# Kernel optimization log

Measured on AMD Instinct MI355X. Metric: run time of the kernel, lower is better.

## Reference

```python
import jax, jax.numpy as jnp
import numpy as np

PI_APPROX = 3.14  # the original module uses 3.14, not math.pi
FPS = 30.0        # hard-coded sampling rate in calc_hr_torch


def setup_inputs() -> dict:
    key = jax.random.key(0)
    x = jax.random.normal(key, (4096, 4096), dtype=jnp.float32)
    return {"x": x}


def reference(x) -> jnp.ndarray:
    test_n, sig_length = x.shape
    # mean-subtract each signal (over last dim)
    x = x - jnp.mean(x, axis=-1, keepdims=True)

    # custom_fft: DFT over dim 0 (size test_n), O(N^2) via trig matmuls
    N = test_n
    n = jnp.arange(N, dtype=jnp.float32)[:, None]  # [N,1]
    k = jnp.arange(N, dtype=jnp.float32)[None, :]  # [1,N]
    ang = (-2.0 * PI_APPROX / N) * (k * n)         # [N,N]
    real_part = jnp.matmul(jnp.cos(ang), x)        # [N, sig_length]
    imag_part = jnp.matmul(jnp.sin(ang), x)

    # custom_rfft: keep non-negative frequencies along dim 0
    half = N // 2 + 1 if N % 2 == 0 else (N + 1) // 2
    real_part = real_part[:half]
    imag_part = imag_part[:half]

    Ns = sig_length
    freq = jnp.arange(Ns, dtype=jnp.float32) / (Ns / FPS)  # [sig_length]
    amplitude = jnp.sqrt(real_part ** 2 + imag_part ** 2) / Ns  # [half, sig_length]
    hr_list = freq[jnp.argmax(amplitude, axis=-1)] * 60.0       # [half]
    return hr_list
```

## Files before the change

kernel.cpp:

```cpp
#include <hip/hip_runtime.h>
#include <cmath>

typedef _Float16 f16;
typedef _Float16 f16x8 __attribute__((ext_vector_type(8)));
typedef float f32x4 __attribute__((ext_vector_type(4)));
typedef unsigned long long u64;

#define M_OUT 2049
#define NDIM 4096
#define MPAD 2112
#define CW ((float)(-2.0 * 3.14 / 4096.0))

static const size_t WS_MEAN  = 0;
static const size_t WS_CELLS = 16384;
static const size_t WS_TBL   = 40960;
static const size_t A_ELEMS  = (size_t)MPAD * NDIM;
static const size_t X_ELEMS  = (size_t)NDIM * NDIM;
static const size_t WS_XTBL  = WS_TBL + 4 * A_ELEMS * sizeof(f16);
static const size_t WS_FULL_END = WS_XTBL + 2 * X_ELEMS * sizeof(f16);
static const size_t WS_MID_END  = WS_TBL + 4 * A_ELEMS * sizeof(f16);

#define AS1 __attribute__((address_space(1)))
#define AS3 __attribute__((address_space(3)))
__device__ __forceinline__ void async_copy16(const void* gsrc, void* ldst) {
    __builtin_amdgcn_global_load_lds((const AS1 unsigned int*)gsrc,
                                     (AS3 unsigned int*)ldst, 16, 0, 0);
}

__device__ __forceinline__ void split_f16(float v, f16& hi, f16& lo) {
    hi = (f16)v;
    lo = (f16)((v - (float)hi) * 64.0f);
}

__global__ void mean_kernel(const float* __restrict__ x, float* __restrict__ meanv,
                            u64* __restrict__ cells) {
    if (blockIdx.x < 9) {
        int i = blockIdx.x * 256 + threadIdx.x;
        if (i < M_OUT) cells[i] = 0ull;
    }
    const int row = blockIdx.x;
    const float4* xr = (const float4*)(x + (size_t)row * NDIM);
    float s = 0.f;
    for (int i = threadIdx.x; i < NDIM / 4; i += 256) {
        float4 v = xr[i];
        s += (v.x + v.y) + (v.z + v.w);
    }
    for (int off = 32; off; off >>= 1) s += __shfl_down(s, off);
    __shared__ float ps[4];
    if ((threadIdx.x & 63) == 0) ps[threadIdx.x >> 6] = s;
    __syncthreads();
    if (threadIdx.x == 0) {
        float t = (ps[0] + ps[1]) + (ps[2] + ps[3]);
        meanv[row] = t * (1.0f / 4096.0f);
    }
}

__global__ void fill_tables_cm(const float* __restrict__ x, const float* __restrict__ meanv,
                               f16* __restrict__ atbl, f16* __restrict__ xtbl) {
    const int c = blockIdx.x;
    if (blockIdx.y < 9) {
        const int m = blockIdx.y * 256 + threadIdx.x;
        if (m >= MPAD) return;
        const bool valid = (m < M_OUT);
        f16x8 chv, clv, shv, slv;
        for (int j = 0; j < 8; ++j) {
            float cc = 0.f, ss = 0.f;
            if (valid) {
                int kk = c * 8 + j;
                float ang = CW * (float)(m * kk);
                sincosf(ang, &ss, &cc);
            }
            f16 h, l;
            split_f16(cc, h, l); chv[j] = h; clv[j] = l;
            split_f16(ss, h, l); shv[j] = h; slv[j] = l;
        }
        size_t idx = ((size_t)c * MPAD + m) * 8;
        *(f16x8*)(atbl + idx)                 = chv;
        *(f16x8*)(atbl + A_ELEMS + idx)       = clv;
        *(f16x8*)(atbl + 2 * A_ELEMS + idx)   = shv;
        *(f16x8*)(atbl + 3 * A_ELEMS + idx)   = slv;
    } else {
        const int n = (blockIdx.y - 9) * 256 + threadIdx.x;
        f16x8 hv, lv;
        for (int j = 0; j < 8; ++j) {
            int k = c * 8 + j;
            float v = x[(size_t)k * NDIM + n] - meanv[k];
            f16 h, l;
            split_f16(v, h, l);
            hv[j] = h; lv[j] = l;
        }
        size_t idx = ((size_t)c * NDIM + n) * 8;
        *(f16x8*)(xtbl + idx)           = hv;
        *(f16x8*)(xtbl + X_ELEMS + idx) = lv;
    }
}

__global__ __launch_bounds__(256, 2) void dft_gemm_cm(
    const f16* __restrict__ atbl, const f16* __restrict__ xtbl,
    u64* __restrict__ cells)
{
    __shared__ alignas(16) f16 sX[3][2][4][128][8];

    const int t = threadIdx.x;
    const int n0 = blockIdx.x * 128;
    const int by = blockIdx.y;

    const int lane = t & 63;
    const int w  = t >> 6;
    const int wm = w >> 1, wn = w & 1;
    const int q  = lane >> 4, ln = lane & 15;

    f32x4 aC0[2][4], aC1[2][4], aS0[2][4], aS1[2][4];

    const int xq0 = w >> 1, xh = w & 1;
    const int xq1 = xq0 + 2;
    const f16* xG0 = xtbl + ((size_t)xq0 * NDIM + n0 + xh * 64 + lane) * 8;
    const f16* xG1 = xtbl + ((size_t)xq1 * NDIM + n0 + xh * 64 + lane) * 8;
    const f16* xG2 = xG0 + X_ELEMS;
    const f16* xG3 = xG1 + X_ELEMS;

    auto stageX = [&](int buf, int kc) {
        const size_t kadv = (size_t)kc * NDIM * 8;
        async_copy16(xG0 + kadv, &sX[buf][0][xq0][xh * 64][0]);
        async_copy16(xG1 + kadv, &sX[buf][0][xq1][xh * 64][0]);
        async_copy16(xG2 + kadv, &sX[buf][1][xq0][xh * 64][0]);
        async_copy16(xG3 + kadv, &sX[buf][1][xq1][xh * 64][0]);
    };

    auto compute = [&](f16x8 (&A)[2][4], int buf) {
        f16x8 bh[4], bl[4];
#pragma unroll
        for (int tn = 0; tn < 4; ++tn) {
            int nl = wn * 64 + tn * 16 + ln;
            bh[tn] = *(const f16x8*)&sX[buf][0][q][nl][0];
            bl[tn] = *(const f16x8*)&sX[buf][1][q][nl][0];
        }
        __builtin_amdgcn_s_setprio(1);
#pragma unroll
        for (int tm = 0; tm < 2; ++tm)
#pragma unroll
            for (int tn = 0; tn < 4; ++tn) {
                aC0[tm][tn] = __builtin_amdgcn_mfma_f32_16x16x32_f16(A[tm][0], bh[tn], aC0[tm][tn], 0, 0, 0);
                aC1[tm][tn] = __builtin_amdgcn_mfma_f32_16x16x32_f16(A[tm][0], bl[tn], aC1[tm][tn], 0, 0, 0);
                aC1[tm][tn] = __builtin_amdgcn_mfma_f32_16x16x32_f16(A[tm][1], bh[tn], aC1[tm][tn], 0, 0, 0);
                aS0[tm][tn] = __builtin_amdgcn_mfma_f32_16x16x32_f16(A[tm][2], bh[tn], aS0[tm][tn], 0, 0, 0);
                aS1[tm][tn] = __builtin_amdgcn_mfma_f32_16x16x32_f16(A[tm][2], bl[tn], aS1[tm][tn], 0, 0, 0);
                aS1[tm][tn] = __builtin_amdgcn_mfma_f32_16x16x32_f16(A[tm][3], bh[tn], aS1[tm][tn], 0, 0, 0);
            }
        __builtin_amdgcn_s_setprio(0);
    };

    f16x8 Aa[2][4], Ab[2][4];

    const int npass = (by == 0) ? 2 : 1;
    for (int pass = 0; pass < npass; ++pass) {
        const int rowBase = (pass == 0) ? by * 64 : 2048;
        __syncthreads();

#pragma unroll
        for (int i = 0; i < 2; ++i)
#pragma unroll
            for (int j = 0; j < 4; ++j) {
                aC0[i][j] = (f32x4){0.f, 0.f, 0.f, 0.f};
                aC1[i][j] = (f32x4){0.f, 0.f, 0.f, 0.f};
                aS0[i][j] = (f32x4){0.f, 0.f, 0.f, 0.f};
                aS1[i][j] = (f32x4){0.f, 0.f, 0.f, 0.f};
            }

        const f16* aBase = atbl + ((size_t)q * MPAD + (rowBase + wm * 32 + ln)) * 8;

        auto loadA = [&](f16x8 (&dst)[2][4], int kc) {
#pragma unroll
            for (int tm = 0; tm < 2; ++tm)
#pragma unroll
                for (int tb = 0; tb < 4; ++tb)
                    dst[tm][tb] = *(const f16x8*)(aBase + (size_t)tb * A_ELEMS
                                  + ((size_t)kc * MPAD + tm * 16) * 8);
        };

        int cur = 0, nxt = 1;
        auto bump = [&]() { cur = nxt; nxt = (nxt == 2) ? 0 : nxt + 1; };

        stageX(0, 0);
        loadA(Aa, 0);

        int kc = 0;
        for (int it = 0; it < 63; ++it) {
            loadA(Ab, kc + 4);
            stageX(nxt, kc + 4);
            asm volatile("s_waitcnt vmcnt(12)" ::: "memory");
            __builtin_amdgcn_s_barrier();
            __builtin_amdgcn_sched_barrier(0);
            compute(Aa, cur);
            bump();
            kc += 4;
            loadA(Aa, kc + 4);
            stageX(nxt, kc + 4);
            asm volatile("s_waitcnt vmcnt(12)" ::: "memory");
            __builtin_amdgcn_s_barrier();
            __builtin_amdgcn_sched_barrier(0);
            compute(Ab, cur);
            bump();
            kc += 4;
        }
        loadA(Ab, kc + 4);
        stageX(nxt, kc + 4);
        asm volatile("s_waitcnt vmcnt(12)" ::: "memory");
        __builtin_amdgcn_s_barrier();
        __builtin_amdgcn_sched_barrier(0);
        compute(Aa, cur);
        bump();
        asm volatile("s_waitcnt vmcnt(0)" ::: "memory");
        __builtin_amdgcn_s_barrier();
        __builtin_amdgcn_sched_barrier(0);
        compute(Ab, cur);

        const float inv64 = 0.015625f;
#pragma unroll
        for (int tm = 0; tm < 2; ++tm) {
#pragma unroll
            for (int r = 0; r < 4; ++r) {
                u64 best = 0ull;
#pragma unroll
                for (int tn = 0; tn < 4; ++tn) {
                    float C = aC0[tm][tn][r] + aC1[tm][tn][r] * inv64;
                    float S = aS0[tm][tn][r] + aS1[tm][tn][r] * inv64;
                    float a2 = C * C + S * S;
                    int col = n0 + wn * 64 + tn * 16 + ln;
                    u64 key = ((u64)__float_as_uint(a2) << 32) | (unsigned)(~col);
                    if (key > best) best = key;
                }
                for (int off = 1; off < 16; off <<= 1) {
                    unsigned hi = (unsigned)(best >> 32), lo = (unsigned)best;
                    unsigned ho = __shfl_xor(hi, off);
                    unsigned lo2 = __shfl_xor(lo, off);
                    u64 o = ((u64)ho << 32) | lo2;
                    if (o > best) best = o;
                }
                if (ln == 0) {
                    int grow = rowBase + wm * 32 + tm * 16 + q * 4 + r;
                    if (grow < M_OUT) atomicMax(cells + grow, best);
                }
            }
        }
    }
}

__global__ void fill_tables_rm(f16* __restrict__ tbl) {
    long long g = (long long)blockIdx.x * 256 + threadIdx.x;
    if (g >= (long long)(MPAD * 512)) return;
    int m  = (int)(g >> 9);
    int kq = ((int)g & 511) * 8;
    bool valid = (m < M_OUT);
    f16x8 chv, clv, shv, slv;
    for (int j = 0; j < 8; ++j) {
        float c = 0.f, s = 0.f;
        if (valid) {
            int kk = kq + j;
            float ang = CW * (float)(m * kk);
            sincosf(ang, &s, &c);
        }
        f16 h, l;
        split_f16(c, h, l); chv[j] = h; clv[j] = l;
        split_f16(s, h, l); shv[j] = h; slv[j] = l;
    }
    size_t idx = (size_t)m * NDIM + kq;
    *(f16x8*)(tbl + idx)               = chv;
    *(f16x8*)(tbl + A_ELEMS + idx)     = clv;
    *(f16x8*)(tbl + 2 * A_ELEMS + idx) = shv;
    *(f16x8*)(tbl + 3 * A_ELEMS + idx) = slv;
}

#define PK 40
__global__ __launch_bounds__(256, 2) void dft_gemm_fb(
    const float* __restrict__ x, const float* __restrict__ meanv,
    const f16* __restrict__ tbl, int useTbl,
    u64* __restrict__ cells)
{
    __shared__ alignas(16) f16 Ach[64][PK];
    __shared__ alignas(16) f16 Acl[64][PK];
    __shared__ alignas(16) f16 Ash[64][PK];
    __shared__ alignas(16) f16 Asl[64][PK];
    __shared__ alignas(16) f16 Xh[128][PK];
    __shared__ alignas(16) f16 Xl[128][PK];

    const int t = threadIdx.x;
    const int n0      = blockIdx.x * 128;
    const int rowBase = blockIdx.y * 64;

    const int am  = t >> 2;
    const int akq = (t & 3) * 8;
    const int xn  = t & 127;
    const int xkh = (t >> 7) * 16;

    const int lane = t & 63;
    const int w  = t >> 6;
    const int wm = w >> 1, wn = w & 1;
    const int q  = lane >> 4, ln = lane & 15;

    f32x4 aC0[2][4], aC1[2][4], aS0[2][4], aS1[2][4];
    for (int i = 0; i < 2; ++i)
        for (int j = 0; j < 4; ++j) {
            aC0[i][j] = (f32x4){0.f, 0.f, 0.f, 0.f};
            aC1[i][j] = (f32x4){0.f, 0.f, 0.f, 0.f};
            aS0[i][j] = (f32x4){0.f, 0.f, 0.f, 0.f};
            aS1[i][j] = (f32x4){0.f, 0.f, 0.f, 0.f};
        }

    const int arow = rowBase + am;
    const bool avalid = (arow < M_OUT);

    for (int k0 = 0; k0 < NDIM; k0 += 32) {
        __syncthreads();
        if (useTbl) {
            size_t idx = (size_t)arow * NDIM + k0 + akq;
            *(f16x8*)&Ach[am][akq] = *(const f16x8*)(tbl + idx);
            *(f16x8*)&Acl[am][akq] = *(const f16x8*)(tbl + A_ELEMS + idx);
            *(f16x8*)&Ash[am][akq] = *(const f16x8*)(tbl + 2 * A_ELEMS + idx);
            *(f16x8*)&Asl[am][akq] = *(const f16x8*)(tbl + 3 * A_ELEMS + idx);
        } else {
            f16x8 chv, clv, shv, slv;
            for (int j = 0; j < 8; ++j) {
                float c = 0.f, s = 0.f;
                if (avalid) {
                    int kk = k0 + akq + j;
                    float ang = CW * (float)(arow * kk);
                    sincosf(ang, &s, &c);
                }
                f16 h, l;
                split_f16(c, h, l); chv[j] = h; clv[j] = l;
                split_f16(s, h, l); shv[j] = h; slv[j] = l;
            }
            *(f16x8*)&Ach[am][akq] = chv;
            *(f16x8*)&Acl[am][akq] = clv;
            *(f16x8*)&Ash[am][akq] = shv;
            *(f16x8*)&Asl[am][akq] = slv;
        }
        {
            const float* xp = x + (size_t)(k0 + xkh) * NDIM + n0 + xn;
            f16x8 h0, h1, l0, l1;
            for (int r = 0; r < 16; ++r) {
                float v = xp[(size_t)r * NDIM] - meanv[k0 + xkh + r];
                f16 hi, lo;
                split_f16(v, hi, lo);
                if (r < 8) { h0[r] = hi; l0[r] = lo; }
                else       { h1[r - 8] = hi; l1[r - 8] = lo; }
            }
            *(f16x8*)&Xh[xn][xkh]     = h0;
            *(f16x8*)&Xh[xn][xkh + 8] = h1;
            *(f16x8*)&Xl[xn][xkh]     = l0;
            *(f16x8*)&Xl[xn][xkh + 8] = l1;
        }
        __syncthreads();
        f16x8 fch[2], fcl[2], fsh[2], fsl[2], bh[4], bl[4];
        for (int tm = 0; tm < 2; ++tm) {
            int ml = wm * 32 + tm * 16 + ln;
            fch[tm] = *(const f16x8*)&Ach[ml][q * 8];
            fcl[tm] = *(const f16x8*)&Acl[ml][q * 8];
            fsh[tm] = *(const f16x8*)&Ash[ml][q * 8];
            fsl[tm] = *(const f16x8*)&Asl[ml][q * 8];
        }
        for (int tn = 0; tn < 4; ++tn) {
            int nl = wn * 64 + tn * 16 + ln;
            bh[tn] = *(const f16x8*)&Xh[nl][q * 8];
            bl[tn] = *(const f16x8*)&Xl[nl][q * 8];
        }
        for (int tm = 0; tm < 2; ++tm)
            for (int tn = 0; tn < 4; ++tn) {
                aC0[tm][tn] = __builtin_amdgcn_mfma_f32_16x16x32_f16(fch[tm], bh[tn], aC0[tm][tn], 0, 0, 0);
                aC1[tm][tn] = __builtin_amdgcn_mfma_f32_16x16x32_f16(fch[tm], bl[tn], aC1[tm][tn], 0, 0, 0);
                aC1[tm][tn] = __builtin_amdgcn_mfma_f32_16x16x32_f16(fcl[tm], bh[tn], aC1[tm][tn], 0, 0, 0);
                aS0[tm][tn] = __builtin_amdgcn_mfma_f32_16x16x32_f16(fsh[tm], bh[tn], aS0[tm][tn], 0, 0, 0);
                aS1[tm][tn] = __builtin_amdgcn_mfma_f32_16x16x32_f16(fsh[tm], bl[tn], aS1[tm][tn], 0, 0, 0);
                aS1[tm][tn] = __builtin_amdgcn_mfma_f32_16x16x32_f16(fsl[tm], bh[tn], aS1[tm][tn], 0, 0, 0);
            }
    }

    const float inv64 = 0.015625f;
    for (int tm = 0; tm < 2; ++tm) {
        for (int r = 0; r < 4; ++r) {
            u64 best = 0ull;
            for (int tn = 0; tn < 4; ++tn) {
                float C = aC0[tm][tn][r] + aC1[tm][tn][r] * inv64;
                float S = aS0[tm][tn][r] + aS1[tm][tn][r] * inv64;
                float a2 = C * C + S * S;
                int col = n0 + wn * 64 + tn * 16 + ln;
                u64 key = ((u64)__float_as_uint(a2) << 32) | (unsigned)(~col);
                if (key > best) best = key;
            }
            for (int off = 1; off < 16; off <<= 1) {
                unsigned hi = (unsigned)(best >> 32), lo = (unsigned)best;
                unsigned ho = __shfl_xor(hi, off);
                unsigned lo2 = __shfl_xor(lo, off);
                u64 o = ((u64)ho << 32) | lo2;
                if (o > best) best = o;
            }
            if (ln == 0) {
                int grow = rowBase + wm * 32 + tm * 16 + q * 4 + r;
                if (grow < M_OUT) atomicMax(cells + grow, best);
            }
        }
    }
}

__global__ void out_kernel(const u64* __restrict__ cells, float* __restrict__ out) {
    int i = blockIdx.x * 256 + threadIdx.x;
    if (i < M_OUT) {
        unsigned col = ~(unsigned)(cells[i] & 0xFFFFFFFFull);
        float freq = (float)col / (4096.0f / 30.0f);
        out[i] = freq * 60.0f;
    }
}

extern "C" void kernel_launch(void* const* d_in, const int* in_sizes, int n_in,
                              void* d_out, int out_size, void* d_ws, size_t ws_size,
                              hipStream_t stream) {
    const float* x = (const float*)d_in[0];
    char* ws = (char*)d_ws;
    float* meanv = (float*)(ws + WS_MEAN);
    u64*   cells = (u64*)(ws + WS_CELLS);
    f16*   atbl  = (f16*)(ws + WS_TBL);
    f16*   xtbl  = (f16*)(ws + WS_XTBL);
    float* out   = (float*)d_out;

    hipLaunchKernelGGL(mean_kernel, dim3(NDIM), dim3(256), 0, stream, x, meanv, cells);

    if (ws_size >= WS_FULL_END) {
        hipLaunchKernelGGL(fill_tables_cm, dim3(512, 25), dim3(256), 0, stream,
                           x, meanv, atbl, xtbl);
        hipLaunchKernelGGL(dft_gemm_cm, dim3(32, 32), dim3(256), 0, stream, atbl, xtbl, cells);
    } else if (ws_size >= WS_MID_END) {
        hipLaunchKernelGGL(fill_tables_rm, dim3(4224), dim3(256), 0, stream, atbl);
        hipLaunchKernelGGL(dft_gemm_fb, dim3(32, 33), dim3(256), 0, stream,
                           x, meanv, atbl, 1, cells);
    } else {
        hipLaunchKernelGGL(dft_gemm_fb, dim3(32, 33), dim3(256), 0, stream,
                           x, meanv, atbl, 0, cells);
    }
    hipLaunchKernelGGL(out_kernel, dim3((M_OUT + 255) / 256), dim3(256), 0, stream, cells, out);
}
```

Measured before the change: 538.6 us.

## Compute Nyquist row in separate fp32 kernels, drop second pass from GEMM blocks

Previously the blockIdx.y==0 blocks of the DFT GEMM ran a second full K pass just to produce output row 2048, so those 32 blocks did twice the work and set the kernel's tail. Row 2048 is now computed by two small kernels, a split-K fp32 partial dot product with sin/cos weights and a reduction plus argmax atomic, launched before the table fill. The partial buffer reuses the table region before the tables are written. The GEMM becomes a single uniform pass per block, which should remove the load imbalance, at the cost of two extra launches and a strided fp32 read of x.

```diff
diff --git a/kernel.cpp b/kernel.cpp
--- a/kernel.cpp
+++ b/kernel.cpp
@@ -53,6 +53,55 @@
         float t = (ps[0] + ps[1]) + (ps[2] + ps[3]);
         meanv[row] = t * (1.0f / 4096.0f);
     }
+}
+
+__global__ __launch_bounds__(256) void nyq_partial(
+    const float* __restrict__ x, const float* __restrict__ meanv,
+    float* __restrict__ part)
+{
+    __shared__ float lc[256], ls[256];
+    __shared__ float sC[128], sS[128];
+    const int t = threadIdx.x;
+    const int ks = blockIdx.y;
+    const int kbase = ks * 256;
+    sincosf(CW * (float)(2048 * (kbase + t)), &ls[t], &lc[t]);
+    __syncthreads();
+    const int col = blockIdx.x * 128 + (t & 127);
+    const int kp  = t >> 7;
+    float C = 0.f, S = 0.f;
+    const float* xp = x + (size_t)(kbase + kp * 128) * NDIM + col;
+    const float* mp = meanv + kbase + kp * 128;
+    for (int i = 0; i < 128; ++i) {
+        float v = xp[(size_t)i * NDIM] - mp[i];
+        C = fmaf(lc[kp * 128 + i], v, C);
+        S = fmaf(ls[kp * 128 + i], v, S);
+    }
+    if (kp) { sC[t - 128] = C; sS[t - 128] = S; }
+    __syncthreads();
+    if (!kp) {
+        part[(size_t)ks * NDIM + col]            = C + sC[t];
+        part[(size_t)(16 + ks) * NDIM + col]     = S + sS[t];
+    }
+}
+
+__global__ __launch_bounds__(256) void nyq_reduce(
+    const float* __restrict__ part, u64* __restrict__ cells)
+{
+    const int n = blockIdx.x * 256 + threadIdx.x;
+    float C = 0.f, S = 0.f;
+    for (int ks = 0; ks < 16; ++ks) {
+        C += part[(size_t)ks * NDIM + n];
+        S += part[(size_t)(16 + ks) * NDIM + n];
+    }
+    float a2 = C * C + S * S;
+    u64 key = ((u64)__float_as_uint(a2) << 32) | (unsigned)(~n);
+    for (int off = 1; off < 64; off <<= 1) {
+        unsigned hi = (unsigned)(key >> 32), lo = (unsigned)key;
+        unsigned ho = __shfl_xor(hi, off), lo2 = __shfl_xor(lo, off);
+        u64 o = ((u64)ho << 32) | lo2;
+        if (o > key) key = o;
+    }
+    if ((threadIdx.x & 63) == 0) atomicMax(cells + 2048, key);
 }
 
 __global__ void fill_tables_cm(const float* __restrict__ x, const float* __restrict__ meanv,
@@ -102,8 +151,8 @@
     __shared__ alignas(16) f16 sX[3][2][4][128][8];
 
     const int t = threadIdx.x;
-    const int n0 = blockIdx.x * 128;
-    const int by = blockIdx.y;
+    const int n0      = blockIdx.x * 128;
+    const int rowBase = blockIdx.y * 64;
 
     const int lane = t & 63;
     const int w  = t >> 6;
@@ -111,6 +160,17 @@
     const int q  = lane >> 4, ln = lane & 15;
 
     f32x4 aC0[2][4], aC1[2][4], aS0[2][4], aS1[2][4];
+#pragma unroll
+    for (int i = 0; i < 2; ++i)
+#pragma unroll
+        for (int j = 0; j < 4; ++j) {
+            aC0[i][j] = (f32x4){0.f, 0.f, 0.f, 0.f};
+            aC1[i][j] = (f32x4){0.f, 0.f, 0.f, 0.f};
+            aS0[i][j] = (f32x4){0.f, 0.f, 0.f, 0.f};
+            aS1[i][j] = (f32x4){0.f, 0.f, 0.f, 0.f};
+        }
+
+    const f16* aBase = atbl + ((size_t)q * MPAD + (rowBase + wm * 32 + ln)) * 8;
 
     const int xq0 = w >> 1, xh = w & 1;
     const int xq1 = xq0 + 2;
@@ -118,6 +178,15 @@
     const f16* xG1 = xtbl + ((size_t)xq1 * NDIM + n0 + xh * 64 + lane) * 8;
     const f16* xG2 = xG0 + X_ELEMS;
     const f16* xG3 = xG1 + X_ELEMS;
+
+    auto loadA = [&](f16x8 (&dst)[2][4], int kc) {
+#pragma unroll
+        for (int tm = 0; tm < 2; ++tm)
+#pragma unroll
+            for (int tb = 0; tb < 4; ++tb)
+                dst[tm][tb] = *(const f16x8*)(aBase + (size_t)tb * A_ELEMS
+                              + ((size_t)kc * MPAD + tm * 16) * 8);
+    };
 
     auto stageX = [&](int buf, int kc) {
         const size_t kadv = (size_t)kc * NDIM * 8;
@@ -151,58 +220,14 @@
     };
 
     f16x8 Aa[2][4], Ab[2][4];
-
-    const int npass = (by == 0) ? 2 : 1;
-    for (int pass = 0; pass < npass; ++pass) {
-        const int rowBase = (pass == 0) ? by * 64 : 2048;
-        __syncthreads();
-
-#pragma unroll
-        for (int i = 0; i < 2; ++i)
-#pragma unroll
-            for (int j = 0; j < 4; ++j) {
-                aC0[i][j] = (f32x4){0.f, 0.f, 0.f, 0.f};
-                aC1[i][j] = (f32x4){0.f, 0.f, 0.f, 0.f};
-                aS0[i][j] = (f32x4){0.f, 0.f, 0.f, 0.f};
-                aS1[i][j] = (f32x4){0.f, 0.f, 0.f, 0.f};
-            }
-
-        const f16* aBase = atbl + ((size_t)q * MPAD + (rowBase + wm * 32 + ln)) * 8;
-
-        auto loadA = [&](f16x8 (&dst)[2][4], int kc) {
-#pragma unroll
-            for (int tm = 0; tm < 2; ++tm)
-#pragma unroll
-                for (int tb = 0; tb < 4; ++tb)
-                    dst[tm][tb] = *(const f16x8*)(aBase + (size_t)tb * A_ELEMS
-                                  + ((size_t)kc * MPAD + tm * 16) * 8);
-        };
-
-        int cur = 0, nxt = 1;
-        auto bump = [&]() { cur = nxt; nxt = (nxt == 2) ? 0 : nxt + 1; };
-
-        stageX(0, 0);
-        loadA(Aa, 0);
-
-        int kc = 0;
-        for (int it = 0; it < 63; ++it) {
-            loadA(Ab, kc + 4);
-            stageX(nxt, kc + 4);
-            asm volatile("s_waitcnt vmcnt(12)" ::: "memory");
-            __builtin_amdgcn_s_barrier();
-            __builtin_amdgcn_sched_barrier(0);
-            compute(Aa, cur);
-            bump();
-            kc += 4;
-            loadA(Aa, kc + 4);
-            stageX(nxt, kc + 4);
-            asm volatile("s_waitcnt vmcnt(12)" ::: "memory");
-            __builtin_amdgcn_s_barrier();
-            __builtin_amdgcn_sched_barrier(0);
-            compute(Ab, cur);
-            bump();
-            kc += 4;
-        }
+    int cur = 0, nxt = 1;
+    auto bump = [&]() { cur = nxt; nxt = (nxt == 2) ? 0 : nxt + 1; };
+
+    stageX(0, 0);
+    loadA(Aa, 0);
+
+    int kc = 0;
+    for (int it = 0; it < 63; ++it) {
         loadA(Ab, kc + 4);
         stageX(nxt, kc + 4);
         asm volatile("s_waitcnt vmcnt(12)" ::: "memory");
@@ -210,37 +235,53 @@
         __builtin_amdgcn_sched_barrier(0);
         compute(Aa, cur);
         bump();
-        asm volatile("s_waitcnt vmcnt(0)" ::: "memory");
+        kc += 4;
+        loadA(Aa, kc + 4);
+        stageX(nxt, kc + 4);
+        asm volatile("s_waitcnt vmcnt(12)" ::: "memory");
         __builtin_amdgcn_s_barrier();
         __builtin_amdgcn_sched_barrier(0);
         compute(Ab, cur);
-
-        const float inv64 = 0.015625f;
-#pragma unroll
-        for (int tm = 0; tm < 2; ++tm) {
-#pragma unroll
-            for (int r = 0; r < 4; ++r) {
-                u64 best = 0ull;
-#pragma unroll
-                for (int tn = 0; tn < 4; ++tn) {
-                    float C = aC0[tm][tn][r] + aC1[tm][tn][r] * inv64;
-                    float S = aS0[tm][tn][r] + aS1[tm][tn][r] * inv64;
-                    float a2 = C * C + S * S;
-                    int col = n0 + wn * 64 + tn * 16 + ln;
-                    u64 key = ((u64)__float_as_uint(a2) << 32) | (unsigned)(~col);
-                    if (key > best) best = key;
-                }
-                for (int off = 1; off < 16; off <<= 1) {
-                    unsigned hi = (unsigned)(best >> 32), lo = (unsigned)best;
-                    unsigned ho = __shfl_xor(hi, off);
-                    unsigned lo2 = __shfl_xor(lo, off);
-                    u64 o = ((u64)ho << 32) | lo2;
-                    if (o > best) best = o;
-                }
-                if (ln == 0) {
-                    int grow = rowBase + wm * 32 + tm * 16 + q * 4 + r;
-                    if (grow < M_OUT) atomicMax(cells + grow, best);
-                }
+        bump();
+        kc += 4;
+    }
+    loadA(Ab, kc + 4);
+    stageX(nxt, kc + 4);
+    asm volatile("s_waitcnt vmcnt(12)" ::: "memory");
+    __builtin_amdgcn_s_barrier();
+    __builtin_amdgcn_sched_barrier(0);
+    compute(Aa, cur);
+    bump();
+    asm volatile("s_waitcnt vmcnt(0)" ::: "memory");
+    __builtin_amdgcn_s_barrier();
+    __builtin_amdgcn_sched_barrier(0);
+    compute(Ab, cur);
+
+    const float inv64 = 0.015625f;
+#pragma unroll
+    for (int tm = 0; tm < 2; ++tm) {
+#pragma unroll
+        for (int r = 0; r < 4; ++r) {
+            u64 best = 0ull;
+#pragma unroll
+            for (int tn = 0; tn < 4; ++tn) {
+                float C = aC0[tm][tn][r] + aC1[tm][tn][r] * inv64;
+                float S = aS0[tm][tn][r] + aS1[tm][tn][r] * inv64;
+                float a2 = C * C + S * S;
+                int col = n0 + wn * 64 + tn * 16 + ln;
+                u64 key = ((u64)__float_as_uint(a2) << 32) | (unsigned)(~col);
+                if (key > best) best = key;
+            }
+            for (int off = 1; off < 16; off <<= 1) {
+                unsigned hi = (unsigned)(best >> 32), lo = (unsigned)best;
+                unsigned ho = __shfl_xor(hi, off);
+                unsigned lo2 = __shfl_xor(lo, off);
+                u64 o = ((u64)ho << 32) | lo2;
+                if (o > best) best = o;
+            }
+            if (ln == 0) {
+                int grow = rowBase + wm * 32 + tm * 16 + q * 4 + r;
+                if (grow < M_OUT) atomicMax(cells + grow, best);
             }
         }
     }
@@ -421,11 +462,14 @@
     u64*   cells = (u64*)(ws + WS_CELLS);
     f16*   atbl  = (f16*)(ws + WS_TBL);
     f16*   xtbl  = (f16*)(ws + WS_XTBL);
+    float* nyqp  = (float*)(ws + WS_TBL);
     float* out   = (float*)d_out;
 
     hipLaunchKernelGGL(mean_kernel, dim3(NDIM), dim3(256), 0, stream, x, meanv, cells);
 
     if (ws_size >= WS_FULL_END) {
+        hipLaunchKernelGGL(nyq_partial, dim3(32, 16), dim3(256), 0, stream, x, meanv, nyqp);
+        hipLaunchKernelGGL(nyq_reduce, dim3(16), dim3(256), 0, stream, nyqp, cells);
         hipLaunchKernelGGL(fill_tables_cm, dim3(512, 25), dim3(256), 0, stream,
                            x, meanv, atbl, xtbl);
         hipLaunchKernelGGL(dft_gemm_cm, dim3(32, 32), dim3(256), 0, stream, atbl, xtbl, cells);
```

Result: faster. 458.0 us (median of 2 runs) (-14.9%).

## Compute Nyquist row separately in fp32 to remove the extra GEMM pass

Applied to the files above, without the earlier changes.

The Nyquist output row (m=2048) is split off from the tensor-core GEMM. Before, block row 0 ran a second full K-loop pass just for that row, so the grid had a straggler. A new mean_nyq kernel computes the row means and, in the same read of x, per-block partial cosine/sine sums for the Nyquist frequency. A small nyq_reduce kernel then sums the partials, subtracts the mean correction, and does the argmax into cells[2048]. The cost is two extra launches and a 16 MB partial buffer that reuses the table region, which is safe only because fill_tables_cm runs afterwards.

```diff
diff --git a/kernel.cpp b/kernel.cpp
--- a/kernel.cpp
+++ b/kernel.cpp
@@ -30,6 +30,101 @@
 __device__ __forceinline__ void split_f16(float v, f16& hi, f16& lo) {
     hi = (f16)v;
     lo = (f16)((v - (float)hi) * 64.0f);
+}
+
+__global__ __launch_bounds__(256) void mean_nyq(
+    const float* __restrict__ x, float* __restrict__ meanv,
+    float* __restrict__ part,
+    u64* __restrict__ cells)
+{
+    const int b = blockIdx.x;
+    const int t = threadIdx.x;
+    if (b < 9) {
+        int i = b * 256 + t;
+        if (i < M_OUT) cells[i] = 0ull;
+    }
+    float lc[8], ls[8];
+#pragma unroll
+    for (int r = 0; r < 8; ++r)
+        sincosf(CW * (float)(2048 * (b * 8 + r)), &ls[r], &lc[r]);
+
+    float C[16], S[16];
+#pragma unroll
+    for (int i = 0; i < 16; ++i) { C[i] = 0.f; S[i] = 0.f; }
+
+    __shared__ float rs[8][4];
+    const int lane = t & 63, w = t >> 6;
+
+    for (int r = 0; r < 8; ++r) {
+        const float4* xr = (const float4*)(x + (size_t)(b * 8 + r) * NDIM);
+        float rsum = 0.f;
+#pragma unroll
+        for (int c = 0; c < 4; ++c) {
+            float4 v = xr[c * 256 + t];
+            rsum += (v.x + v.y) + (v.z + v.w);
+            C[c*4+0] = fmaf(lc[r], v.x, C[c*4+0]);  S[c*4+0] = fmaf(ls[r], v.x, S[c*4+0]);
+            C[c*4+1] = fmaf(lc[r], v.y, C[c*4+1]);  S[c*4+1] = fmaf(ls[r], v.y, S[c*4+1]);
+            C[c*4+2] = fmaf(lc[r], v.z, C[c*4+2]);  S[c*4+2] = fmaf(ls[r], v.z, S[c*4+2]);
+            C[c*4+3] = fmaf(lc[r], v.w, C[c*4+3]);  S[c*4+3] = fmaf(ls[r], v.w, S[c*4+3]);
+        }
+        for (int off = 32; off; off >>= 1) rsum += __shfl_down(rsum, off);
+        if (lane == 0) rs[r][w] = rsum;
+    }
+    __syncthreads();
+    if (t < 8) {
+        float s = (rs[t][0] + rs[t][1]) + (rs[t][2] + rs[t][3]);
+        meanv[b * 8 + t] = s * (1.0f / 4096.0f);
+    }
+#pragma unroll
+    for (int c = 0; c < 4; ++c) {
+        int col = 4 * (c * 256 + t);
+        float4 pc = { C[c*4+0], C[c*4+1], C[c*4+2], C[c*4+3] };
+        float4 ps = { S[c*4+0], S[c*4+1], S[c*4+2], S[c*4+3] };
+        *(float4*)(part + (size_t)b * NDIM + col)         = pc;
+        *(float4*)(part + (size_t)(512 + b) * NDIM + col) = ps;
+    }
+}
+
+__global__ __launch_bounds__(256) void nyq_reduce(
+    const float* __restrict__ part, const float* __restrict__ meanv,
+    u64* __restrict__ cells)
+{
+    const int t = threadIdx.x;
+    float cc = 0.f, cs = 0.f;
+#pragma unroll
+    for (int j = 0; j < 16; ++j) {
+        int k = t * 16 + j;
+        float s, c;
+        sincosf(CW * (float)(2048 * k), &s, &c);
+        float m = meanv[k];
+        cc = fmaf(c, m, cc);
+        cs = fmaf(s, m, cs);
+    }
+    __shared__ float sc[256], ss[256];
+    sc[t] = cc; ss[t] = cs;
+    __syncthreads();
+    for (int off = 128; off; off >>= 1) {
+        if (t < off) { sc[t] += sc[t + off]; ss[t] += ss[t + off]; }
+        __syncthreads();
+    }
+    const float corrC = sc[0], corrS = ss[0];
+
+    const int n = blockIdx.x * 256 + t;
+    float C = 0.f, S = 0.f;
+    for (int b = 0; b < 512; ++b) {
+        C += part[(size_t)b * NDIM + n];
+        S += part[(size_t)(512 + b) * NDIM + n];
+    }
+    C -= corrC; S -= corrS;
+    float a2 = C * C + S * S;
+    u64 key = ((u64)__float_as_uint(a2) << 32) | (unsigned)(~n);
+    for (int off = 1; off < 64; off <<= 1) {
+        unsigned hi = (unsigned)(key >> 32), lo = (unsigned)key;
+        unsigned ho = __shfl_xor(hi, off), lo2 = __shfl_xor(lo, off);
+        u64 o = ((u64)ho << 32) | lo2;
+        if (o > key) key = o;
+    }
+    if ((t & 63) == 0) atomicMax(cells + 2048, key);
 }
 
 __global__ void mean_kernel(const float* __restrict__ x, float* __restrict__ meanv,
@@ -102,8 +197,8 @@
     __shared__ alignas(16) f16 sX[3][2][4][128][8];
 
     const int t = threadIdx.x;
-    const int n0 = blockIdx.x * 128;
-    const int by = blockIdx.y;
+    const int n0      = blockIdx.x * 128;
+    const int rowBase = blockIdx.y * 64;
 
     const int lane = t & 63;
     const int w  = t >> 6;
@@ -111,6 +206,17 @@
     const int q  = lane >> 4, ln = lane & 15;
 
     f32x4 aC0[2][4], aC1[2][4], aS0[2][4], aS1[2][4];
+#pragma unroll
+    for (int i = 0; i < 2; ++i)
+#pragma unroll
+        for (int j = 0; j < 4; ++j) {
+            aC0[i][j] = (f32x4){0.f, 0.f, 0.f, 0.f};
+            aC1[i][j] = (f32x4){0.f, 0.f, 0.f, 0.f};
+            aS0[i][j] = (f32x4){0.f, 0.f, 0.f, 0.f};
+            aS1[i][j] = (f32x4){0.f, 0.f, 0.f, 0.f};
+        }
+
+    const f16* aBase = atbl + ((size_t)q * MPAD + (rowBase + wm * 32 + ln)) * 8;
 
     const int xq0 = w >> 1, xh = w & 1;
     const int xq1 = xq0 + 2;
@@ -118,6 +224,15 @@
     const f16* xG1 = xtbl + ((size_t)xq1 * NDIM + n0 + xh * 64 + lane) * 8;
     const f16* xG2 = xG0 + X_ELEMS;
     const f16* xG3 = xG1 + X_ELEMS;
+
+    auto loadA = [&](f16x8 (&dst)[2][4], int kc) {
+#pragma unroll
+        for (int tm = 0; tm < 2; ++tm)
+#pragma unroll
+            for (int tb = 0; tb < 4; ++tb)
+                dst[tm][tb] = *(const f16x8*)(aBase + (size_t)tb * A_ELEMS
+                              + ((size_t)kc * MPAD + tm * 16) * 8);
+    };
 
     auto stageX = [&](int buf, int kc) {
         const size_t kadv = (size_t)kc * NDIM * 8;
@@ -151,58 +266,14 @@
     };
 
     f16x8 Aa[2][4], Ab[2][4];
-
-    const int npass = (by == 0) ? 2 : 1;
-    for (int pass = 0; pass < npass; ++pass) {
-        const int rowBase = (pass == 0) ? by * 64 : 2048;
-        __syncthreads();
-
-#pragma unroll
-        for (int i = 0; i < 2; ++i)
-#pragma unroll
-            for (int j = 0; j < 4; ++j) {
-                aC0[i][j] = (f32x4){0.f, 0.f, 0.f, 0.f};
-                aC1[i][j] = (f32x4){0.f, 0.f, 0.f, 0.f};
-                aS0[i][j] = (f32x4){0.f, 0.f, 0.f, 0.f};
-                aS1[i][j] = (f32x4){0.f, 0.f, 0.f, 0.f};
-            }
-
-        const f16* aBase = atbl + ((size_t)q * MPAD + (rowBase + wm * 32 + ln)) * 8;
-
-        auto loadA = [&](f16x8 (&dst)[2][4], int kc) {
-#pragma unroll
-            for (int tm = 0; tm < 2; ++tm)
-#pragma unroll
-                for (int tb = 0; tb < 4; ++tb)
-                    dst[tm][tb] = *(const f16x8*)(aBase + (size_t)tb * A_ELEMS
-                                  + ((size_t)kc * MPAD + tm * 16) * 8);
-        };
-
-        int cur = 0, nxt = 1;
-        auto bump = [&]() { cur = nxt; nxt = (nxt == 2) ? 0 : nxt + 1; };
-
-        stageX(0, 0);
-        loadA(Aa, 0);
-
-        int kc = 0;
-        for (int it = 0; it < 63; ++it) {
-            loadA(Ab, kc + 4);
-            stageX(nxt, kc + 4);
-            asm volatile("s_waitcnt vmcnt(12)" ::: "memory");
-            __builtin_amdgcn_s_barrier();
-            __builtin_amdgcn_sched_barrier(0);
-            compute(Aa, cur);
-            bump();
-            kc += 4;
-            loadA(Aa, kc + 4);
-            stageX(nxt, kc + 4);
-            asm volatile("s_waitcnt vmcnt(12)" ::: "memory");
-            __builtin_amdgcn_s_barrier();
-            __builtin_amdgcn_sched_barrier(0);
-            compute(Ab, cur);
-            bump();
-            kc += 4;
-        }
+    int cur = 0, nxt = 1;
+    auto bump = [&]() { cur = nxt; nxt = (nxt == 2) ? 0 : nxt + 1; };
+
+    stageX(0, 0);
+    loadA(Aa, 0);
+
+    int kc = 0;
+    for (int it = 0; it < 63; ++it) {
         loadA(Ab, kc + 4);
         stageX(nxt, kc + 4);
         asm volatile("s_waitcnt vmcnt(12)" ::: "memory");
@@ -210,37 +281,53 @@
         __builtin_amdgcn_sched_barrier(0);
         compute(Aa, cur);
         bump();
-        asm volatile("s_waitcnt vmcnt(0)" ::: "memory");
+        kc += 4;
+        loadA(Aa, kc + 4);
+        stageX(nxt, kc + 4);
+        asm volatile("s_waitcnt vmcnt(12)" ::: "memory");
         __builtin_amdgcn_s_barrier();
         __builtin_amdgcn_sched_barrier(0);
         compute(Ab, cur);
-
-        const float inv64 = 0.015625f;
-#pragma unroll
-        for (int tm = 0; tm < 2; ++tm) {
-#pragma unroll
-            for (int r = 0; r < 4; ++r) {
-                u64 best = 0ull;
-#pragma unroll
-                for (int tn = 0; tn < 4; ++tn) {
-                    float C = aC0[tm][tn][r] + aC1[tm][tn][r] * inv64;
-                    float S = aS0[tm][tn][r] + aS1[tm][tn][r] * inv64;
-                    float a2 = C * C + S * S;
-                    int col = n0 + wn * 64 + tn * 16 + ln;
-                    u64 key = ((u64)__float_as_uint(a2) << 32) | (unsigned)(~col);
-                    if (key > best) best = key;
-                }
-                for (int off = 1; off < 16; off <<= 1) {
-                    unsigned hi = (unsigned)(best >> 32), lo = (unsigned)best;
-                    unsigned ho = __shfl_xor(hi, off);
-                    unsigned lo2 = __shfl_xor(lo, off);
-                    u64 o = ((u64)ho << 32) | lo2;
-                    if (o > best) best = o;
-                }
-                if (ln == 0) {
-                    int grow = rowBase + wm * 32 + tm * 16 + q * 4 + r;
-                    if (grow < M_OUT) atomicMax(cells + grow, best);
-                }
+        bump();
+        kc += 4;
+    }
+    loadA(Ab, kc + 4);
+    stageX(nxt, kc + 4);
+    asm volatile("s_waitcnt vmcnt(12)" ::: "memory");
+    __builtin_amdgcn_s_barrier();
+    __builtin_amdgcn_sched_barrier(0);
+    compute(Aa, cur);
+    bump();
+    asm volatile("s_waitcnt vmcnt(0)" ::: "memory");
+    __builtin_amdgcn_s_barrier();
+    __builtin_amdgcn_sched_barrier(0);
+    compute(Ab, cur);
+
+    const float inv64 = 0.015625f;
+#pragma unroll
+    for (int tm = 0; tm < 2; ++tm) {
+#pragma unroll
+        for (int r = 0; r < 4; ++r) {
+            u64 best = 0ull;
+#pragma unroll
+            for (int tn = 0; tn < 4; ++tn) {
+                float C = aC0[tm][tn][r] + aC1[tm][tn][r] * inv64;
+                float S = aS0[tm][tn][r] + aS1[tm][tn][r] * inv64;
+                float a2 = C * C + S * S;
+                int col = n0 + wn * 64 + tn * 16 + ln;
+                u64 key = ((u64)__float_as_uint(a2) << 32) | (unsigned)(~col);
+                if (key > best) best = key;
+            }
+            for (int off = 1; off < 16; off <<= 1) {
+                unsigned hi = (unsigned)(best >> 32), lo = (unsigned)best;
+                unsigned ho = __shfl_xor(hi, off);
+                unsigned lo2 = __shfl_xor(lo, off);
+                u64 o = ((u64)ho << 32) | lo2;
+                if (o > best) best = o;
+            }
+            if (ln == 0) {
+                int grow = rowBase + wm * 32 + tm * 16 + q * 4 + r;
+                if (grow < M_OUT) atomicMax(cells + grow, best);
             }
         }
     }
@@ -421,19 +508,22 @@
     u64*   cells = (u64*)(ws + WS_CELLS);
     f16*   atbl  = (f16*)(ws + WS_TBL);
     f16*   xtbl  = (f16*)(ws + WS_XTBL);
+    float* nyqp  = (float*)(ws + WS_TBL);
     float* out   = (float*)d_out;
 
-    hipLaunchKernelGGL(mean_kernel, dim3(NDIM), dim3(256), 0, stream, x, meanv, cells);
-
     if (ws_size >= WS_FULL_END) {
+        hipLaunchKernelGGL(mean_nyq, dim3(512), dim3(256), 0, stream, x, meanv, nyqp, cells);
+        hipLaunchKernelGGL(nyq_reduce, dim3(16), dim3(256), 0, stream, nyqp, meanv, cells);
         hipLaunchKernelGGL(fill_tables_cm, dim3(512, 25), dim3(256), 0, stream,
                            x, meanv, atbl, xtbl);
         hipLaunchKernelGGL(dft_gemm_cm, dim3(32, 32), dim3(256), 0, stream, atbl, xtbl, cells);
     } else if (ws_size >= WS_MID_END) {
+        hipLaunchKernelGGL(mean_kernel, dim3(NDIM), dim3(256), 0, stream, x, meanv, cells);
         hipLaunchKernelGGL(fill_tables_rm, dim3(4224), dim3(256), 0, stream, atbl);
         hipLaunchKernelGGL(dft_gemm_fb, dim3(32, 33), dim3(256), 0, stream,
                            x, meanv, atbl, 1, cells);
     } else {
+        hipLaunchKernelGGL(mean_kernel, dim3(NDIM), dim3(256), 0, stream, x, meanv, cells);
         hipLaunchKernelGGL(dft_gemm_fb, dim3(32, 33), dim3(256), 0, stream,
                            x, meanv, atbl, 0, cells);
     }
```

Result: faster. 488.9 us (-9.2%).
